# Performance work log

Hardware: AMD Instinct MI355X
Metric: run time of the kernel (lower is better)

Reference implementation:

```python
import jax, jax.numpy as jnp
import numpy as np

C_M, C_Z, C_H = 256, 128, 32
LN_EPS = 1e-5


def setup_inputs() -> dict:
    key = jax.random.key(0)
    ks = jax.random.split(key, 8)
    B, N_SEQ, S = 1, 128, 256
    m = jax.random.normal(ks[0], (B, N_SEQ, S, C_M), dtype=jnp.float32)
    ln_w = jnp.ones((C_M,), jnp.float32)
    ln_b = jnp.zeros((C_M,), jnp.float32)
    Wa = jax.random.normal(ks[1], (C_M, C_H), jnp.float32) / np.sqrt(C_M)
    ba = jnp.zeros((C_H,), jnp.float32)
    Wb = jax.random.normal(ks[2], (C_M, C_H), jnp.float32) / np.sqrt(C_M)
    bb = jnp.zeros((C_H,), jnp.float32)
    Wo = jax.random.normal(ks[3], (C_H * C_H, C_Z), jnp.float32) / np.sqrt(C_H * C_H)
    bo = jnp.zeros((C_Z,), jnp.float32)
    return {"m": m, "ln_w": ln_w, "ln_b": ln_b, "Wa": Wa, "ba": ba,
            "Wb": Wb, "bb": bb, "Wo": Wo, "bo": bo}


def reference(m, ln_w, ln_b, Wa, ba, Wb, bb, Wo, bo):
    B, n_seq, S, _ = m.shape
    # LayerNorm over c_m
    mu = jnp.mean(m, axis=-1, keepdims=True)
    var = jnp.var(m, axis=-1, keepdims=True)
    mn = (m - mu) * jax.lax.rsqrt(var + LN_EPS) * ln_w + ln_b
    # dual projections: [B, n_seq, S, c_hidden]
    a = mn @ Wa + ba
    b = mn @ Wb + bb
    # outer product mean contracted over MSA rows s: [B, S, S, c_h, c_h]
    outer = jnp.einsum('bsic,bsjd->bijcd', a, b) / n_seq
    outer = outer.reshape(B, S, S, C_H * C_H)
    z_update = outer @ Wo + bo  # [B, S, S, c_z]
    return z_update
```

## Files before the change

kernel.cpp:

```cpp
#include <hip/hip_runtime.h>
#include <stdint.h>

#define NS 128
#define NR 256
#define CM 256
#define CH 32
#define CZ 128

typedef __attribute__((ext_vector_type(4))) float f32x4;
typedef __attribute__((ext_vector_type(8))) short bf16x8;
typedef __attribute__((ext_vector_type(4))) unsigned short u16x4;

__device__ __forceinline__ unsigned short bf16rne(float x) {
    unsigned int u = __builtin_bit_cast(unsigned int, x);
    return (unsigned short)((u + 0x7FFFu + ((u >> 16) & 1u)) >> 16);
}

__global__ __launch_bounds__(256) void k_wrepack(const float* __restrict__ Wa,
                                                 const float* __restrict__ Wb,
                                                 const float* __restrict__ Wo,
                                                 unsigned short* __restrict__ Wab_f,
                                                 unsigned short* __restrict__ Wo_f) {
    int idx = blockIdx.x * 256 + threadIdx.x;
    int l = idx & 63;
    int lo = l & 15, hi = l >> 4;
    if (idx < 2048) {
        int ks = (idx >> 6) & 7;
        int n = idx >> 9;
        int k = n * 16 + lo;
        bf16x8 v;
#pragma unroll
        for (int e = 0; e < 8; ++e) {
            int c = ks * 32 + hi * 8 + e;
            float wv = (k < CH) ? Wa[c * CH + k] : Wb[c * CH + (k - CH)];
            v[e] = (short)bf16rne(wv);
        }
        *reinterpret_cast<bf16x8*>(Wab_f + (size_t)idx * 8) = v;
    } else if (idx < 2048 + 16384) {
        int t = idx - 2048;
        int kt = (t >> 6) & 7;
        int c = t >> 9;
        int k = kt * 16 + lo;
        bf16x8 v;
#pragma unroll
        for (int e = 0; e < 8; ++e) {
            int d = hi * 8 + e;
            v[e] = (short)bf16rne(Wo[(size_t)(c * 32 + d) * CZ + k]);
        }
        *reinterpret_cast<bf16x8*>(Wo_f + (size_t)t * 8) = v;
    }
}

__global__ __launch_bounds__(256) void k_lnproj(const float* __restrict__ m,
                                                const float* __restrict__ lnw,
                                                const float* __restrict__ lnb,
                                                const float* __restrict__ ba,
                                                const float* __restrict__ bb,
                                                const unsigned short* __restrict__ Wab_f,
                                                unsigned short* __restrict__ a_n,
                                                unsigned short* __restrict__ b_n) {
    __shared__ unsigned short mn_lds[64 * 256];
    const int tid = threadIdx.x, l = tid & 63, w = tid >> 6;
    const int lo = l & 15, hi = l >> 4;
    const int R0 = blockIdx.x * 64;

    float4 wv = *reinterpret_cast<const float4*>(lnw + l * 4);
    float4 bv = *reinterpret_cast<const float4*>(lnb + l * 4);

    for (int t = 0; t < 16; ++t) {
        int row = w * 16 + t;
        int gr = R0 + row;
        float4 x = *reinterpret_cast<const float4*>(m + (size_t)gr * CM + l * 4);
        float sum = x.x + x.y + x.z + x.w;
        float sq = x.x * x.x + x.y * x.y + x.z * x.z + x.w * x.w;
#pragma unroll
        for (int off = 32; off; off >>= 1) {
            sum += __shfl_xor(sum, off);
            sq  += __shfl_xor(sq, off);
        }
        float mu = sum * (1.f / CM);
        float rstd = rsqrtf(sq * (1.f / CM) - mu * mu + 1e-5f);
        u16x4 pk;
        pk[0] = bf16rne((x.x - mu) * rstd * wv.x + bv.x);
        pk[1] = bf16rne((x.y - mu) * rstd * wv.y + bv.y);
        pk[2] = bf16rne((x.z - mu) * rstd * wv.z + bv.z);
        pk[3] = bf16rne((x.w - mu) * rstd * wv.w + bv.w);
        int byte = row * 512 + l * 8;
        byte ^= (row & 7) << 4;
        *reinterpret_cast<u16x4*>(reinterpret_cast<char*>(mn_lds) + byte) = pk;
    }

    f32x4 acc[4];
#pragma unroll
    for (int n = 0; n < 4; ++n) acc[n] = (f32x4){0.f, 0.f, 0.f, 0.f};
    const int arow = w * 16 + lo;
#pragma unroll
    for (int ks = 0; ks < 8; ++ks) {
        int byte = arow * 512 + ks * 64 + hi * 16;
        byte ^= (arow & 7) << 4;
        bf16x8 afrag = *reinterpret_cast<const bf16x8*>(reinterpret_cast<const char*>(mn_lds) + byte);
#pragma unroll
        for (int n = 0; n < 4; ++n) {
            bf16x8 bfrag = *reinterpret_cast<const bf16x8*>(Wab_f + (size_t)((n * 8 + ks) * 64 + l) * 8);
            acc[n] = __builtin_amdgcn_mfma_f32_16x16x32_bf16(afrag, bfrag, acc[n], 0, 0, 0);
        }
    }
#pragma unroll
    for (int n = 0; n < 4; ++n) {
        int k = n * 16 + lo;
        float bias = (k < CH) ? ba[k] : bb[k - CH];
#pragma unroll
        for (int r = 0; r < 4; ++r) {
            int gr = R0 + w * 16 + hi * 4 + r;
            unsigned short hv = bf16rne(acc[n][r] + bias);
            if (k < CH) a_n[(size_t)gr * CH + k] = hv;
            else        b_n[(size_t)gr * CH + (k - CH)] = hv;
        }
    }
}

__global__ __launch_bounds__(256) void k_abrepack(const unsigned short* __restrict__ a_n,
                                                  const unsigned short* __restrict__ b_n,
                                                  unsigned short* __restrict__ a_f,
                                                  unsigned short* __restrict__ b_f) {
    int idx = blockIdx.x * 256 + threadIdx.x;
    int lo = idx & 15, hi = (idx >> 4) & 3;
    if (idx < 131072) {
        int ks = (idx >> 6) & 3, it = (idx >> 8) & 15, c = idx >> 12;
        int i = it * 16 + lo;
        bf16x8 v;
#pragma unroll
        for (int e = 0; e < 8; ++e) {
            int s = ks * 32 + hi * 8 + e;
            v[e] = (short)a_n[((size_t)s * NR + i) * CH + c];
        }
        *reinterpret_cast<bf16x8*>(a_f + (size_t)idx * 8) = v;
    } else {
        int t = idx - 131072;
        int ks = (t >> 6) & 3, tt = t >> 8;
        int j = tt >> 1, d = (tt & 1) * 16 + lo;
        bf16x8 v;
#pragma unroll
        for (int e = 0; e < 8; ++e) {
            int s = ks * 32 + hi * 8 + e;
            v[e] = (short)b_n[((size_t)s * NR + j) * CH + d];
        }
        *reinterpret_cast<bf16x8*>(b_f + (size_t)t * 8) = v;
    }
}

__global__ __launch_bounds__(256, 2) void k_outer(const unsigned short* __restrict__ a_f,
                                                  const unsigned short* __restrict__ b_f,
                                                  const unsigned short* __restrict__ Wo_f,
                                                  const float* __restrict__ bo,
                                                  float* __restrict__ out) {
    __shared__ unsigned short b_lds[32768];
    __shared__ unsigned short O_lds[2][4096];
    const int tid = threadIdx.x, l = tid & 63, w = tid >> 6;
    const int lo = l & 15, hi = l >> 4;
    const int bi = blockIdx.x >> 5, bj = blockIdx.x & 31;

    {
        const unsigned short* src = b_f + (size_t)bj * 32768;
#pragma unroll
        for (int it = 0; it < 16; ++it) {
            int off = it * 2048 + tid * 8;
            *reinterpret_cast<bf16x8*>(b_lds + off) =
                *reinterpret_cast<const bf16x8*>(src + off);
        }
    }
    __syncthreads();

    f32x4 zacc[2][8];
#pragma unroll
    for (int jj = 0; jj < 2; ++jj)
#pragma unroll
        for (int kt = 0; kt < 8; ++kt)
            zacc[jj][kt] = (f32x4){0.f, 0.f, 0.f, 0.f};

#pragma unroll 2
    for (int c = 0; c < 32; ++c) {
        bf16x8 wof[8];
#pragma unroll
        for (int kt = 0; kt < 8; ++kt)
            wof[kt] = *reinterpret_cast<const bf16x8*>(Wo_f + (size_t)((c * 8 + kt) * 64 + l) * 8);
        bf16x8 af[4];
#pragma unroll
        for (int ks = 0; ks < 4; ++ks)
            af[ks] = *reinterpret_cast<const bf16x8*>(a_f + (size_t)(((c * 16 + bi) * 4 + ks) * 64 + l) * 8);

#pragma unroll
        for (int q = 0; q < 4; ++q) {
            f32x4 o = (f32x4){0.f, 0.f, 0.f, 0.f};
#pragma unroll
            for (int ks = 0; ks < 4; ++ks) {
                bf16x8 bfrag = *reinterpret_cast<const bf16x8*>(
                    b_lds + (size_t)(((w * 4 + q) * 4 + ks) * 64 + l) * 8);
                o = __builtin_amdgcn_mfma_f32_16x16x32_bf16(bfrag, af[ks], o, 0, 0, 0);
            }
            u16x4 pk;
            pk[0] = bf16rne(o[0]); pk[1] = bf16rne(o[1]);
            pk[2] = bf16rne(o[2]); pk[3] = bf16rne(o[3]);
            int byte = (lo << 9) + (w * 4 + q) * 32 + (hi << 3);
            byte ^= (lo & 7) << 4;
            *reinterpret_cast<u16x4*>(reinterpret_cast<char*>(O_lds[c & 1]) + byte) = pk;
        }

#pragma unroll
        for (int jj = 0; jj < 2; ++jj) {
            int rbyte = (lo << 9) + w * 128 + jj * 64 + (hi << 4);
            rbyte ^= (lo & 7) << 4;
            bf16x8 ofrag = *reinterpret_cast<const bf16x8*>(
                reinterpret_cast<const char*>(O_lds[c & 1]) + rbyte);
#pragma unroll
            for (int kt = 0; kt < 8; ++kt)
                zacc[jj][kt] = __builtin_amdgcn_mfma_f32_16x16x32_bf16(ofrag, wof[kt], zacc[jj][kt], 0, 0, 0);
        }
    }

#pragma unroll
    for (int jj = 0; jj < 2; ++jj) {
        int j = bj * 8 + w * 2 + jj;
#pragma unroll
        for (int kt = 0; kt < 8; ++kt) {
            int k = kt * 16 + lo;
            float bok = bo[k];
#pragma unroll
            for (int r = 0; r < 4; ++r) {
                int i = bi * 16 + hi * 4 + r;
                out[((size_t)i * NR + j) * CZ + k] = zacc[jj][kt][r] * (1.f / NS) + bok;
            }
        }
    }
}

extern "C" void kernel_launch(void* const* d_in, const int* in_sizes, int n_in,
                              void* d_out, int out_size, void* d_ws, size_t ws_size,
                              hipStream_t stream) {
    const float* m   = (const float*)d_in[0];
    const float* lnw = (const float*)d_in[1];
    const float* lnb = (const float*)d_in[2];
    const float* Wa  = (const float*)d_in[3];
    const float* ba  = (const float*)d_in[4];
    const float* Wb  = (const float*)d_in[5];
    const float* bb  = (const float*)d_in[6];
    const float* Wo  = (const float*)d_in[7];
    const float* bo  = (const float*)d_in[8];
    float* out = (float*)d_out;

    unsigned short* ws    = (unsigned short*)d_ws;
    unsigned short* a_n   = ws;
    unsigned short* b_n   = ws + 1048576;
    unsigned short* a_f   = ws + 2097152;
    unsigned short* b_f   = ws + 3145728;
    unsigned short* Wab_f = ws + 4194304;
    unsigned short* Wo_f  = ws + 4210688;
    const size_t WS_NEEDED = (size_t)(4210688 + 131072) * 2;
    if (ws_size < WS_NEEDED) return;

    k_wrepack<<<72, 256, 0, stream>>>(Wa, Wb, Wo, Wab_f, Wo_f);
    k_lnproj<<<512, 256, 0, stream>>>(m, lnw, lnb, ba, bb, Wab_f, a_n, b_n);
    k_abrepack<<<1024, 256, 0, stream>>>(a_n, b_n, a_f, b_f);
    k_outer<<<512, 256, 0, stream>>>(a_f, b_f, Wo_f, bo, out);
}
```

Before: 64.71 us.

## Switch outer-product kernel to 32x32x16 MFMA with register-shuffled intermediate

Rewrites k_outer to use 32x32x16 bf16 MFMA tiles with 512-thread blocks, each wave owning one j column and 32 rows of i. The per-c intermediate outer-product tile is no longer staged through double-buffered LDS. It is packed to bf16 and exchanged between half-waves with shuffles, then fed straight into the Wo projection MFMAs. The b fragments are hoisted into registers once per block, and the a/b/Wo repack layouts change to match the new MFMA operand shapes. The cost is higher register pressure from 16-wide accumulators and a grid of half as many blocks, which may lower occupancy.

After: 81.76 us. 26.3% more time.

```diff
diff --git a/kernel.cpp b/kernel.cpp
--- a/kernel.cpp
+++ b/kernel.cpp
@@ -8,12 +8,18 @@
 #define CZ 128
 
 typedef __attribute__((ext_vector_type(4))) float f32x4;
+typedef __attribute__((ext_vector_type(16))) float f32x16;
 typedef __attribute__((ext_vector_type(8))) short bf16x8;
 typedef __attribute__((ext_vector_type(4))) unsigned short u16x4;
+typedef __attribute__((ext_vector_type(4))) unsigned int u32x4;
 
 __device__ __forceinline__ unsigned short bf16rne(float x) {
     unsigned int u = __builtin_bit_cast(unsigned int, x);
     return (unsigned short)((u + 0x7FFFu + ((u >> 16) & 1u)) >> 16);
+}
+
+__device__ __forceinline__ unsigned int pack2_bf16(float lo, float hi) {
+    return (unsigned int)bf16rne(lo) | ((unsigned int)bf16rne(hi) << 16);
 }
 
 __global__ __launch_bounds__(256) void k_wrepack(const float* __restrict__ Wa,
@@ -24,6 +30,7 @@
     int idx = blockIdx.x * 256 + threadIdx.x;
     int l = idx & 63;
     int lo = l & 15, hi = l >> 4;
+    int il = l & 31, h = l >> 5;
     if (idx < 2048) {
         int ks = (idx >> 6) & 7;
         int n = idx >> 9;
@@ -38,14 +45,12 @@
         *reinterpret_cast<bf16x8*>(Wab_f + (size_t)idx * 8) = v;
     } else if (idx < 2048 + 16384) {
         int t = idx - 2048;
-        int kt = (t >> 6) & 7;
-        int c = t >> 9;
-        int k = kt * 16 + lo;
-        bf16x8 v;
-#pragma unroll
-        for (int e = 0; e < 8; ++e) {
-            int d = hi * 8 + e;
-            v[e] = (short)bf16rne(Wo[(size_t)(c * 32 + d) * CZ + k]);
+        int ks2 = (t >> 6) & 1, kt = (t >> 7) & 3, c = t >> 9;
+        bf16x8 v;
+#pragma unroll
+        for (int e = 0; e < 8; ++e) {
+            int d = ks2 * 16 + h * 8 + e;
+            v[e] = (short)bf16rne(Wo[(size_t)(c * 32 + d) * CZ + kt * 32 + il]);
         }
         *reinterpret_cast<bf16x8*>(Wo_f + (size_t)t * 8) = v;
     }
@@ -124,112 +129,126 @@
                                                   unsigned short* __restrict__ a_f,
                                                   unsigned short* __restrict__ b_f) {
     int idx = blockIdx.x * 256 + threadIdx.x;
-    int lo = idx & 15, hi = (idx >> 4) & 3;
+    int l = idx & 63, il = l & 31, h = (l >> 5) & 1;
     if (idx < 131072) {
-        int ks = (idx >> 6) & 3, it = (idx >> 8) & 15, c = idx >> 12;
-        int i = it * 16 + lo;
-        bf16x8 v;
-#pragma unroll
-        for (int e = 0; e < 8; ++e) {
-            int s = ks * 32 + hi * 8 + e;
+        int ks = (idx >> 6) & 7, ib = (idx >> 9) & 7, c = idx >> 12;
+        int i = ib * 32 + il;
+        bf16x8 v;
+#pragma unroll
+        for (int e = 0; e < 8; ++e) {
+            int s = ks * 16 + h * 8 + e;
             v[e] = (short)a_n[((size_t)s * NR + i) * CH + c];
         }
         *reinterpret_cast<bf16x8*>(a_f + (size_t)idx * 8) = v;
     } else {
         int t = idx - 131072;
-        int ks = (t >> 6) & 3, tt = t >> 8;
-        int j = tt >> 1, d = (tt & 1) * 16 + lo;
-        bf16x8 v;
-#pragma unroll
-        for (int e = 0; e < 8; ++e) {
-            int s = ks * 32 + hi * 8 + e;
-            v[e] = (short)b_n[((size_t)s * NR + j) * CH + d];
+        int ks = (t >> 6) & 7, jl = (t >> 9) & 7, jb = t >> 12;
+        int j = jb * 8 + jl;
+        bf16x8 v;
+#pragma unroll
+        for (int e = 0; e < 8; ++e) {
+            int s = ks * 16 + h * 8 + e;
+            v[e] = (short)b_n[((size_t)s * NR + j) * CH + il];
         }
         *reinterpret_cast<bf16x8*>(b_f + (size_t)t * 8) = v;
     }
 }
 
-__global__ __launch_bounds__(256, 2) void k_outer(const unsigned short* __restrict__ a_f,
-                                                  const unsigned short* __restrict__ b_f,
-                                                  const unsigned short* __restrict__ Wo_f,
-                                                  const float* __restrict__ bo,
-                                                  float* __restrict__ out) {
+__global__ __launch_bounds__(512) void k_outer(const unsigned short* __restrict__ a_f,
+                                               const unsigned short* __restrict__ b_f,
+                                               const unsigned short* __restrict__ Wo_f,
+                                               const float* __restrict__ bo,
+                                               float* __restrict__ out) {
     __shared__ unsigned short b_lds[32768];
-    __shared__ unsigned short O_lds[2][4096];
     const int tid = threadIdx.x, l = tid & 63, w = tid >> 6;
-    const int lo = l & 15, hi = l >> 4;
+    const int il = l & 31, h = l >> 5;
     const int bi = blockIdx.x >> 5, bj = blockIdx.x & 31;
 
     {
         const unsigned short* src = b_f + (size_t)bj * 32768;
 #pragma unroll
-        for (int it = 0; it < 16; ++it) {
-            int off = it * 2048 + tid * 8;
+        for (int it = 0; it < 8; ++it) {
+            int off = it * 4096 + tid * 8;
             *reinterpret_cast<bf16x8*>(b_lds + off) =
                 *reinterpret_cast<const bf16x8*>(src + off);
         }
     }
     __syncthreads();
 
-    f32x4 zacc[2][8];
-#pragma unroll
-    for (int jj = 0; jj < 2; ++jj)
-#pragma unroll
-        for (int kt = 0; kt < 8; ++kt)
-            zacc[jj][kt] = (f32x4){0.f, 0.f, 0.f, 0.f};
+    bf16x8 bfr[8];
+#pragma unroll
+    for (int ks = 0; ks < 8; ++ks)
+        bfr[ks] = *reinterpret_cast<const bf16x8*>(b_lds + ((w * 8 + ks) * 64 + l) * 8);
+
+    f32x16 zacc[4];
+#pragma unroll
+    for (int kt = 0; kt < 4; ++kt)
+        zacc[kt] = (f32x16){0.f,0.f,0.f,0.f,0.f,0.f,0.f,0.f,0.f,0.f,0.f,0.f,0.f,0.f,0.f,0.f};
 
 #pragma unroll 2
     for (int c = 0; c < 32; ++c) {
-        bf16x8 wof[8];
-#pragma unroll
-        for (int kt = 0; kt < 8; ++kt)
-            wof[kt] = *reinterpret_cast<const bf16x8*>(Wo_f + (size_t)((c * 8 + kt) * 64 + l) * 8);
-        bf16x8 af[4];
-#pragma unroll
-        for (int ks = 0; ks < 4; ++ks)
-            af[ks] = *reinterpret_cast<const bf16x8*>(a_f + (size_t)(((c * 16 + bi) * 4 + ks) * 64 + l) * 8);
-
-#pragma unroll
-        for (int q = 0; q < 4; ++q) {
-            f32x4 o = (f32x4){0.f, 0.f, 0.f, 0.f};
-#pragma unroll
-            for (int ks = 0; ks < 4; ++ks) {
-                bf16x8 bfrag = *reinterpret_cast<const bf16x8*>(
-                    b_lds + (size_t)(((w * 4 + q) * 4 + ks) * 64 + l) * 8);
-                o = __builtin_amdgcn_mfma_f32_16x16x32_bf16(bfrag, af[ks], o, 0, 0, 0);
-            }
-            u16x4 pk;
-            pk[0] = bf16rne(o[0]); pk[1] = bf16rne(o[1]);
-            pk[2] = bf16rne(o[2]); pk[3] = bf16rne(o[3]);
-            int byte = (lo << 9) + (w * 4 + q) * 32 + (hi << 3);
-            byte ^= (lo & 7) << 4;
-            *reinterpret_cast<u16x4*>(reinterpret_cast<char*>(O_lds[c & 1]) + byte) = pk;
-        }
-
-#pragma unroll
-        for (int jj = 0; jj < 2; ++jj) {
-            int rbyte = (lo << 9) + w * 128 + jj * 64 + (hi << 4);
-            rbyte ^= (lo & 7) << 4;
-            bf16x8 ofrag = *reinterpret_cast<const bf16x8*>(
-                reinterpret_cast<const char*>(O_lds[c & 1]) + rbyte);
-#pragma unroll
-            for (int kt = 0; kt < 8; ++kt)
-                zacc[jj][kt] = __builtin_amdgcn_mfma_f32_16x16x32_bf16(ofrag, wof[kt], zacc[jj][kt], 0, 0, 0);
-        }
-    }
-
-#pragma unroll
-    for (int jj = 0; jj < 2; ++jj) {
-        int j = bj * 8 + w * 2 + jj;
-#pragma unroll
-        for (int kt = 0; kt < 8; ++kt) {
-            int k = kt * 16 + lo;
-            float bok = bo[k];
-#pragma unroll
-            for (int r = 0; r < 4; ++r) {
-                int i = bi * 16 + hi * 4 + r;
-                out[((size_t)i * NR + j) * CZ + k] = zacc[jj][kt][r] * (1.f / NS) + bok;
-            }
+        bf16x8 af[8];
+#pragma unroll
+        for (int ks = 0; ks < 8; ++ks)
+            af[ks] = *reinterpret_cast<const bf16x8*>(a_f + (size_t)(((c * 8 + bi) * 8 + ks) * 64 + l) * 8);
+        bf16x8 wof0[4], wof1[4];
+#pragma unroll
+        for (int kt = 0; kt < 4; ++kt) {
+            wof0[kt] = *reinterpret_cast<const bf16x8*>(Wo_f + (size_t)(((c * 4 + kt) * 2 + 0) * 64 + l) * 8);
+            wof1[kt] = *reinterpret_cast<const bf16x8*>(Wo_f + (size_t)(((c * 4 + kt) * 2 + 1) * 64 + l) * 8);
+        }
+
+        f32x16 o = (f32x16){0.f,0.f,0.f,0.f,0.f,0.f,0.f,0.f,0.f,0.f,0.f,0.f,0.f,0.f,0.f,0.f};
+#pragma unroll
+        for (int ks = 0; ks < 8; ++ks)
+            o = __builtin_amdgcn_mfma_f32_32x32x16_bf16(bfr[ks], af[ks], o, 0, 0, 0);
+
+        unsigned int u0 = pack2_bf16(o[0],  o[1]);
+        unsigned int u1 = pack2_bf16(o[2],  o[3]);
+        unsigned int u2 = pack2_bf16(o[4],  o[5]);
+        unsigned int u3 = pack2_bf16(o[6],  o[7]);
+        unsigned int u4 = pack2_bf16(o[8],  o[9]);
+        unsigned int u5 = pack2_bf16(o[10], o[11]);
+        unsigned int u6 = pack2_bf16(o[12], o[13]);
+        unsigned int u7 = pack2_bf16(o[14], o[15]);
+        unsigned int p0 = __shfl_xor(u0, 32);
+        unsigned int p1 = __shfl_xor(u1, 32);
+        unsigned int p2 = __shfl_xor(u2, 32);
+        unsigned int p3 = __shfl_xor(u3, 32);
+        unsigned int p4 = __shfl_xor(u4, 32);
+        unsigned int p5 = __shfl_xor(u5, 32);
+        unsigned int p6 = __shfl_xor(u6, 32);
+        unsigned int p7 = __shfl_xor(u7, 32);
+        u32x4 t0 = h ? (u32x4){p0, p1, u0, u1} : (u32x4){u0, u1, p0, p1};
+        u32x4 t1 = h ? (u32x4){p2, p3, u2, u3} : (u32x4){u2, u3, p2, p3};
+        u32x4 t2 = h ? (u32x4){p4, p5, u4, u5} : (u32x4){u4, u5, p4, p5};
+        u32x4 t3 = h ? (u32x4){p6, p7, u6, u7} : (u32x4){u6, u7, p6, p7};
+        bf16x8 pa0 = __builtin_bit_cast(bf16x8, t0);
+        bf16x8 pa1 = __builtin_bit_cast(bf16x8, t1);
+        bf16x8 pa2 = __builtin_bit_cast(bf16x8, t2);
+        bf16x8 pa3 = __builtin_bit_cast(bf16x8, t3);
+
+        f32x4 dummy;
+        u32x4 lo16 = h ? (u32x4){t1[0], t1[1], t1[2], t1[3]} : (u32x4){t0[0], t0[1], t0[2], t0[3]};
+        u32x4 hi16 = h ? (u32x4){t3[0], t3[1], t3[2], t3[3]} : (u32x4){t2[0], t2[1], t2[2], t2[3]};
+        bf16x8 paA = __builtin_bit_cast(bf16x8, lo16);
+        bf16x8 paB = __builtin_bit_cast(bf16x8, hi16);
+#pragma unroll
+        for (int kt = 0; kt < 4; ++kt) {
+            zacc[kt] = __builtin_amdgcn_mfma_f32_32x32x16_bf16(paA, wof0[kt], zacc[kt], 0, 0, 0);
+            zacc[kt] = __builtin_amdgcn_mfma_f32_32x32x16_bf16(paB, wof1[kt], zacc[kt], 0, 0, 0);
+        }
+        (void)dummy; (void)pa0; (void)pa1; (void)pa2; (void)pa3;
+    }
+
+    const int j = bj * 8 + w;
+#pragma unroll
+    for (int kt = 0; kt < 4; ++kt) {
+        float bok = bo[kt * 32 + il];
+#pragma unroll
+        for (int r = 0; r < 16; ++r) {
+            int i = bi * 32 + (r & 3) + 8 * (r >> 2) + 4 * h;
+            out[((size_t)i * NR + j) * CZ + kt * 32 + il] = zacc[kt][r] * (1.f / NS) + bok;
         }
     }
 }
@@ -261,5 +280,5 @@
     k_wrepack<<<72, 256, 0, stream>>>(Wa, Wb, Wo, Wab_f, Wo_f);
     k_lnproj<<<512, 256, 0, stream>>>(m, lnw, lnb, ba, bb, Wab_f, a_n, b_n);
     k_abrepack<<<1024, 256, 0, stream>>>(a_n, b_n, a_f, b_f);
-    k_outer<<<512, 256, 0, stream>>>(a_f, b_f, Wo_f, bo, out);
-}
+    k_outer<<<256, 512, 0, stream>>>(a_f, b_f, Wo_f, bo, out);
+}
```
